# Optimization experiments

Hardware: AMD Instinct MI355X
Metric: run time of the kernel (lower is better)

The kernel has to match this reference:

```python
import jax, jax.numpy as jnp
import numpy as np

B, T, C = 4, 2048, 1024
NH, HS = 16, 64  # num_heads, head_size; NH*HS == C


def setup_inputs() -> dict:
    key = jax.random.key(0)
    ks = jax.random.split(key, 6)
    scale = C ** -0.5
    return {
        "x": jax.random.normal(ks[0], (B, T, C), dtype=jnp.float32),
        "Wk": jax.random.normal(ks[1], (C, C), dtype=jnp.float32) * scale,
        "Wq": jax.random.normal(ks[2], (C, C), dtype=jnp.float32) * scale,
        "Wv": jax.random.normal(ks[3], (C, C), dtype=jnp.float32) * scale,
        "Wp": jax.random.normal(ks[4], (C, C), dtype=jnp.float32) * scale,
        "bp": jax.random.normal(ks[5], (C,), dtype=jnp.float32) * 0.01,
    }


def reference(x, Wk, Wq, Wv, Wp, bp):
    # x: [B, T, C]. Linear(y) = y @ W.T (torch convention), no bias for k/q/v.
    def split_heads(t):
        return t.reshape(B, T, NH, HS).transpose(0, 2, 1, 3)  # [B, NH, T, HS]

    k = split_heads(x @ Wk.T)
    q = split_heads(x @ Wq.T)
    v = split_heads(x @ Wv.T)

    scores = jnp.einsum('bnqh,bnkh->bnqk', q, k) * (HS ** -0.5)  # [B,NH,T,T]
    causal = jnp.tril(jnp.ones((T, T), dtype=bool))
    scores = jnp.where(causal[None, None, :, :], scores, -jnp.inf)
    att = jax.nn.softmax(scores, axis=-1)
    out = jnp.einsum('bnqk,bnkh->bnqh', att, v)  # [B,NH,T,HS]
    out = out.transpose(0, 2, 1, 3).reshape(B, T, C)
    out = out @ Wp.T + bp
    return out
```

## Files before the change

kernel.cpp:

```cpp
#include <hip/hip_runtime.h>
#include <hip/hip_bf16.h>
#include <stdint.h>

typedef unsigned int uint;
typedef unsigned short ushort_t;
typedef unsigned long long ull;

#define B_ 4
#define T_ 2048
#define C_ 1024
#define NH_ 16
#define HS_ 64
#define M_ (B_*T_)

typedef __bf16 bf16x8 __attribute__((ext_vector_type(8)));
typedef float f32x4 __attribute__((ext_vector_type(4)));

__device__ __forceinline__ ushort_t f2bf(float f) {
    uint u = __builtin_bit_cast(uint, f);
    u += 0x7fff + ((u >> 16) & 1);
    return (ushort_t)(u >> 16);
}

__device__ __forceinline__ void gload_lds16(const void* g, void* l) {
    __builtin_amdgcn_global_load_lds((const __attribute__((address_space(1))) void*)g,
                                     (__attribute__((address_space(3))) void*)l, 16, 0, 0);
}

__global__ void convert_bf16(const float* __restrict__ in, ushort_t* __restrict__ out,
                             int n4) {
    int i = blockIdx.x * blockDim.x + threadIdx.x;
    if (i >= n4) return;
    float4 v = ((const float4*)in)[i];
    ushort4 o;
    o.x = f2bf(v.x); o.y = f2bf(v.y); o.z = f2bf(v.z); o.w = f2bf(v.w);
    ((ushort4*)out)[i] = o;
}

__global__ void convert_w4(const float* __restrict__ Wq, const float* __restrict__ Wk,
                           const float* __restrict__ Wv, const float* __restrict__ Wp,
                           ushort_t* __restrict__ wqkv, ushort_t* __restrict__ wp) {
    int i = blockIdx.x * blockDim.x + threadIdx.x;
    int which = blockIdx.y;
    const float* src = (which == 0) ? Wq : (which == 1) ? Wk : (which == 2) ? Wv : Wp;
    ushort_t* dst = (which < 3) ? (wqkv + (size_t)which * C_ * C_) : wp;
    float scale = (which == 0) ? 0.125f * 1.44269504088896f : 1.0f;
    float4 v = ((const float4*)src)[i];
    ushort4 o;
    o.x = f2bf(v.x * scale); o.y = f2bf(v.y * scale);
    o.z = f2bf(v.z * scale); o.w = f2bf(v.w * scale);
    ((ushort4*)dst)[i] = o;
}

template<int MODE>
__global__ __launch_bounds__(256) void gemm_nt(const ushort_t* __restrict__ A,
                                               const ushort_t* __restrict__ Bw,
                                               void* __restrict__ out0,
                                               ushort_t* __restrict__ out1,
                                               ushort_t* __restrict__ out2,
                                               const float* __restrict__ bias) {
    __shared__ __align__(16) ushort_t As[128 * 32];
    __shared__ __align__(16) ushort_t Bs[128 * 32];

    const int tid  = threadIdx.x;
    const int lane = tid & 63;
    const int w    = tid >> 6;
    const int wm   = w >> 1, wn = w & 1;
    const int r16  = lane & 15, g = lane >> 4;
    const int row0 = blockIdx.y * 128;
    const int col0 = blockIdx.x * 128;

    f32x4 acc[4][4] = {};

    for (int kt = 0; kt < C_ / 32; ++kt) {
        const int k0 = kt * 32;
#pragma unroll
        for (int i = 0; i < 2; ++i) {
            int s = i * 256 + w * 64 + lane;
            const ushort_t* ga = A  + (size_t)(row0 + (s >> 2)) * C_ + k0 + (s & 3) * 8;
            const ushort_t* gb = Bw + (size_t)(col0 + (s >> 2)) * C_ + k0 + (s & 3) * 8;
            gload_lds16(ga, &As[(i * 256 + w * 64) * 8]);
            gload_lds16(gb, &Bs[(i * 256 + w * 64) * 8]);
        }
        __syncthreads();

        bf16x8 af[4], bfr[4];
#pragma unroll
        for (int m = 0; m < 4; ++m)
            af[m] = *reinterpret_cast<const bf16x8*>(&As[(wm * 64 + m * 16 + r16) * 32 + g * 8]);
#pragma unroll
        for (int n = 0; n < 4; ++n)
            bfr[n] = *reinterpret_cast<const bf16x8*>(&Bs[(wn * 64 + n * 16 + r16) * 32 + g * 8]);
#pragma unroll
        for (int m = 0; m < 4; ++m)
#pragma unroll
            for (int n = 0; n < 4; ++n)
                acc[m][n] = __builtin_amdgcn_mfma_f32_16x16x32_bf16(af[m], bfr[n], acc[m][n], 0, 0, 0);
        __syncthreads();
    }

#pragma unroll
    for (int m = 0; m < 4; ++m) {
#pragma unroll
        for (int n = 0; n < 4; ++n) {
#pragma unroll
            for (int r = 0; r < 4; ++r) {
                int row = row0 + wm * 64 + m * 16 + g * 4 + r;
                int col = col0 + wn * 64 + n * 16 + r16;
                float val = acc[m][n][r];
                if (MODE == 2) {
                    ((float*)out0)[(size_t)row * C_ + col] = val + bias[col];
                } else {
                    int b = row >> 11, t = row & (T_ - 1);
                    int sect = col >> 10;
                    int c = col & (C_ - 1);
                    int h = c >> 6, hs = c & 63;
                    size_t bh = (size_t)(b * NH_ + h);
                    if (sect == 0)
                        ((ushort_t*)out0)[(bh * T_ + t) * HS_ + hs] = f2bf(val);
                    else if (sect == 1)
                        out1[(bh * T_ + t) * HS_ + hs] = f2bf(val);
                    else
                        out2[(bh * HS_ + hs) * T_ + t] = f2bf(val);
                }
            }
        }
    }
}

__global__ __launch_bounds__(512) void attn_fwd(const ushort_t* __restrict__ q,
                                                const ushort_t* __restrict__ k,
                                                const ushort_t* __restrict__ vT,
                                                ushort_t* __restrict__ o) {
    __shared__ __align__(16) ushort_t Kt[2][64 * 64];
    __shared__ __align__(16) ushort_t Vt[2][64 * 64];
    __shared__ __align__(16) ushort_t Pl[8][16 * 64];

    const int tid  = threadIdx.x;
    const int lane = tid & 63;
    const int w    = tid >> 6;
    const int r16  = lane & 15, g = lane >> 4;
    const int bid  = blockIdx.x;
    const int bh   = bid & 63;
    const int qt   = (T_ / 128 - 1) - (bid >> 6);
    const int qw   = qt * 128 + w * 16;
    const int nt   = 2 * qt + 2;

    const size_t hbase = (size_t)bh * T_ * HS_;

    bf16x8 qf[2];
#pragma unroll
    for (int s = 0; s < 2; ++s)
        qf[s] = *reinterpret_cast<const bf16x8*>(&q[hbase + (size_t)(qw + r16) * HS_ + s * 32 + g * 8]);

    f32x4 oacc[4] = {};
    float lrow[4] = {0.f, 0.f, 0.f, 0.f};

    {
        int s = tid, rr = s >> 3, j = s & 7, jg = j ^ (rr & 7);
        gload_lds16(k  + hbase + (size_t)rr * HS_ + jg * 8, &Kt[0][s * 8]);
        gload_lds16(vT + hbase + (size_t)rr * T_  + jg * 8, &Vt[0][s * 8]);
    }

    for (int kt = 0; kt < nt; ++kt) {
        const int cur = kt & 1;
        const int kb  = kt * 64;

        if (kt + 1 < nt) {
            int kb2 = kb + 64;
            int s = tid, rr = s >> 3, j = s & 7, jg = j ^ (rr & 7);
            gload_lds16(k  + hbase + (size_t)(kb2 + rr) * HS_ + jg * 8, &Kt[cur ^ 1][s * 8]);
            gload_lds16(vT + hbase + (size_t)rr * T_ + kb2 + jg * 8,    &Vt[cur ^ 1][s * 8]);
            asm volatile("s_waitcnt vmcnt(2)" ::: "memory");
        } else {
            asm volatile("s_waitcnt vmcnt(0)" ::: "memory");
        }
        __builtin_amdgcn_s_barrier();
        asm volatile("" ::: "memory");

        if (kb <= qw + 15) {
            f32x4 sacc[4] = {};
            __builtin_amdgcn_s_setprio(1);
#pragma unroll
            for (int n = 0; n < 4; ++n) {
#pragma unroll
                for (int s = 0; s < 2; ++s) {
                    int rowk = n * 16 + r16;
                    int cb = (s * 64 + g * 16) ^ ((rowk & 7) << 4);
                    bf16x8 kf = *reinterpret_cast<const bf16x8*>(
                        reinterpret_cast<const char*>(&Kt[cur][rowk * 64]) + cb);
                    sacc[n] = __builtin_amdgcn_mfma_f32_16x16x32_bf16(qf[s], kf, sacc[n], 0, 0, 0);
                }
            }
            __builtin_amdgcn_s_setprio(0);

            const bool need_mask = (kb + 63 > qw);
            ushort_t* pb = &Pl[w][0];
#pragma unroll
            for (int n = 0; n < 4; ++n) {
#pragma unroll
                for (int r = 0; r < 4; ++r) {
                    float sv = sacc[n][r];
                    if (need_mask) {
                        int kcol = kb + n * 16 + r16;
                        int qrow = qw + g * 4 + r;
                        if (kcol > qrow) sv = -1e30f;
                    }
                    float p = __builtin_amdgcn_exp2f(sv);
                    lrow[r] += p;
                    ushort_t pb16 = (ushort_t)((__builtin_bit_cast(uint, p) + 0x8000u) >> 16);
                    int prow = g * 4 + r;
                    int cb = (n * 32 + r16 * 2) ^ ((prow & 7) << 4);
                    *(ushort_t*)((char*)pb + prow * 128 + cb) = pb16;
                }
            }

            __builtin_amdgcn_s_setprio(1);
#pragma unroll
            for (int s = 0; s < 2; ++s) {
                int cbp = (s * 64 + g * 16) ^ ((r16 & 7) << 4);
                bf16x8 pf = *reinterpret_cast<const bf16x8*>((const char*)pb + r16 * 128 + cbp);
#pragma unroll
                for (int n = 0; n < 4; ++n) {
                    int rowv = n * 16 + r16;
                    int cbv = (s * 64 + g * 16) ^ ((rowv & 7) << 4);
                    bf16x8 vf = *reinterpret_cast<const bf16x8*>(
                        reinterpret_cast<const char*>(&Vt[cur][rowv * 64]) + cbv);
                    oacc[n] = __builtin_amdgcn_mfma_f32_16x16x32_bf16(pf, vf, oacc[n], 0, 0, 0);
                }
            }
            __builtin_amdgcn_s_setprio(0);
        }
        __builtin_amdgcn_s_barrier();
        asm volatile("" ::: "memory");
    }

#pragma unroll
    for (int mk = 1; mk <= 8; mk <<= 1)
#pragma unroll
        for (int r = 0; r < 4; ++r)
            lrow[r] += __shfl_xor(lrow[r], mk, 64);

    const int b = bh >> 4, h = bh & 15;
#pragma unroll
    for (int r = 0; r < 4; ++r) {
        float inv = 1.0f / lrow[r];
        int trow = qw + g * 4 + r;
        size_t obase = ((size_t)(b * T_ + trow) << 10) + h * 64;
#pragma unroll
        for (int n = 0; n < 4; ++n)
            o[obase + n * 16 + r16] = f2bf(oacc[n][r] * inv);
    }
}

extern "C" void kernel_launch(void* const* d_in, const int* in_sizes, int n_in,
                              void* d_out, int out_size, void* d_ws, size_t ws_size,
                              hipStream_t stream) {
    const float* x  = (const float*)d_in[0];
    const float* Wk = (const float*)d_in[1];
    const float* Wq = (const float*)d_in[2];
    const float* Wv = (const float*)d_in[3];
    const float* Wp = (const float*)d_in[4];
    const float* bp = (const float*)d_in[5];
    float* out = (float*)d_out;

    char* ws = (char*)d_ws;
    ushort_t* xbf  = (ushort_t*)(ws);
    ushort_t* wqkv = (ushort_t*)(ws + (size_t)(16 << 20));
    ushort_t* wpbf = (ushort_t*)(ws + (size_t)(22 << 20));
    ushort_t* qb   = (ushort_t*)(ws + (size_t)(24 << 20));
    ushort_t* kb   = (ushort_t*)(ws + (size_t)(40 << 20));
    ushort_t* vtb  = (ushort_t*)(ws + (size_t)(56 << 20));
    ushort_t* aob  = (ushort_t*)(ws + (size_t)(72 << 20));

    {
        int n4 = M_ * C_ / 4;
        convert_bf16<<<dim3((n4 + 255) / 256), dim3(256), 0, stream>>>(x, xbf, n4);
    }
    {
        int n4 = C_ * C_ / 4;
        convert_w4<<<dim3(n4 / 256, 4), dim3(256), 0, stream>>>(Wq, Wk, Wv, Wp, wqkv, wpbf);
    }

    gemm_nt<0><<<dim3(3 * C_ / 128, M_ / 128), 256, 0, stream>>>(xbf, wqkv, qb, kb, vtb, nullptr);

    attn_fwd<<<dim3((T_ / 128) * B_ * NH_), 512, 0, stream>>>(qb, kb, vtb, aob);

    gemm_nt<2><<<dim3(C_ / 128, M_ / 128), 256, 0, stream>>>(aob, wpbf, out, nullptr, nullptr, bp);
}
```

Baseline: 269.3 us.

## Double-buffer GEMM with 128x256 tiles, BK=64, swizzled LDS and 512 threads

Rewrites the bf16 NT GEMM main loop used for both the QKV and output projections. Tiles grow to 128x256 with K-step 64 and 8 waves per block. Global-to-LDS loads for the next K tile are issued before computing on the current one, gated by vmcnt waits and raw barriers. LDS uses an XOR swizzle to avoid bank conflicts, and s_setprio is raised around the MFMA burst. The aim is to hide load latency and cut barriers per FLOP, at the cost of 96KB of LDS per block, which lowers occupancy, and fewer blocks for the output projection.

```diff
diff --git a/kernel.cpp b/kernel.cpp
--- a/kernel.cpp
+++ b/kernel.cpp
@@ -25,6 +25,10 @@
 __device__ __forceinline__ void gload_lds16(const void* g, void* l) {
     __builtin_amdgcn_global_load_lds((const __attribute__((address_space(1))) void*)g,
                                      (__attribute__((address_space(3))) void*)l, 16, 0, 0);
+}
+
+__device__ __forceinline__ f32x4 mfma16(bf16x8 a, bf16x8 b, f32x4 c) {
+    return __builtin_amdgcn_mfma_f32_16x16x32_bf16(a, b, c, 0, 0, 0);
 }
 
 __global__ void convert_bf16(const float* __restrict__ in, ushort_t* __restrict__ out,
@@ -53,50 +57,89 @@
 }
 
 template<int MODE>
-__global__ __launch_bounds__(256) void gemm_nt(const ushort_t* __restrict__ A,
+__global__ __launch_bounds__(512) void gemm_nt(const ushort_t* __restrict__ A,
                                                const ushort_t* __restrict__ Bw,
                                                void* __restrict__ out0,
                                                ushort_t* __restrict__ out1,
                                                ushort_t* __restrict__ out2,
                                                const float* __restrict__ bias) {
-    __shared__ __align__(16) ushort_t As[128 * 32];
-    __shared__ __align__(16) ushort_t Bs[128 * 32];
+    __shared__ __align__(16) ushort_t As[2][128 * 64];
+    __shared__ __align__(16) ushort_t Bs[2][256 * 64];
 
     const int tid  = threadIdx.x;
     const int lane = tid & 63;
     const int w    = tid >> 6;
-    const int wm   = w >> 1, wn = w & 1;
+    const int wm   = w >> 2;
+    const int wn   = w & 3;
     const int r16  = lane & 15, g = lane >> 4;
     const int row0 = blockIdx.y * 128;
-    const int col0 = blockIdx.x * 128;
+    const int col0 = blockIdx.x * 256;
+    const int NK   = C_ / 64;
 
     f32x4 acc[4][4] = {};
 
-    for (int kt = 0; kt < C_ / 32; ++kt) {
-        const int k0 = kt * 32;
-#pragma unroll
-        for (int i = 0; i < 2; ++i) {
-            int s = i * 256 + w * 64 + lane;
-            const ushort_t* ga = A  + (size_t)(row0 + (s >> 2)) * C_ + k0 + (s & 3) * 8;
-            const ushort_t* gb = Bw + (size_t)(col0 + (s >> 2)) * C_ + k0 + (s & 3) * 8;
-            gload_lds16(ga, &As[(i * 256 + w * 64) * 8]);
-            gload_lds16(gb, &Bs[(i * 256 + w * 64) * 8]);
+#pragma unroll
+    for (int i = 0; i < 2; ++i) {
+        int s = i * 512 + tid, row = s >> 3, jg = (s & 7) ^ (row & 7);
+        gload_lds16(A + (size_t)(row0 + row) * C_ + jg * 8, &As[0][s * 8]);
+    }
+#pragma unroll
+    for (int i = 0; i < 4; ++i) {
+        int s = i * 512 + tid, row = s >> 3, jg = (s & 7) ^ (row & 7);
+        gload_lds16(Bw + (size_t)(col0 + row) * C_ + jg * 8, &Bs[0][s * 8]);
+    }
+
+    for (int kt = 0; kt < NK; ++kt) {
+        const int cur = kt & 1;
+        if (kt + 1 < NK) {
+            const int k0 = (kt + 1) * 64;
+#pragma unroll
+            for (int i = 0; i < 2; ++i) {
+                int s = i * 512 + tid, row = s >> 3, jg = (s & 7) ^ (row & 7);
+                gload_lds16(A + (size_t)(row0 + row) * C_ + k0 + jg * 8, &As[cur ^ 1][s * 8]);
+            }
+#pragma unroll
+            for (int i = 0; i < 4; ++i) {
+                int s = i * 512 + tid, row = s >> 3, jg = (s & 7) ^ (row & 7);
+                gload_lds16(Bw + (size_t)(col0 + row) * C_ + k0 + jg * 8, &Bs[cur ^ 1][s * 8]);
+            }
+            asm volatile("s_waitcnt vmcnt(6)" ::: "memory");
+        } else {
+            asm volatile("s_waitcnt vmcnt(0)" ::: "memory");
         }
-        __syncthreads();
-
-        bf16x8 af[4], bfr[4];
+        __builtin_amdgcn_s_barrier();
+        asm volatile("" ::: "memory");
+
+        const char* Ab = (const char*)&As[cur][0];
+        const char* Bb = (const char*)&Bs[cur][0];
+        bf16x8 af[4][2], bfr[4][2];
 #pragma unroll
         for (int m = 0; m < 4; ++m)
-            af[m] = *reinterpret_cast<const bf16x8*>(&As[(wm * 64 + m * 16 + r16) * 32 + g * 8]);
+#pragma unroll
+            for (int sk = 0; sk < 2; ++sk) {
+                int row = wm * 64 + m * 16 + r16;
+                int j = ((sk * 4 + g) ^ (r16 & 7)) * 16;
+                af[m][sk] = *(const bf16x8*)(Ab + row * 128 + j);
+            }
 #pragma unroll
         for (int n = 0; n < 4; ++n)
-            bfr[n] = *reinterpret_cast<const bf16x8*>(&Bs[(wn * 64 + n * 16 + r16) * 32 + g * 8]);
+#pragma unroll
+            for (int sk = 0; sk < 2; ++sk) {
+                int row = wn * 64 + n * 16 + r16;
+                int j = ((sk * 4 + g) ^ (r16 & 7)) * 16;
+                bfr[n][sk] = *(const bf16x8*)(Bb + row * 128 + j);
+            }
+        __builtin_amdgcn_s_setprio(1);
 #pragma unroll
         for (int m = 0; m < 4; ++m)
 #pragma unroll
-            for (int n = 0; n < 4; ++n)
-                acc[m][n] = __builtin_amdgcn_mfma_f32_16x16x32_bf16(af[m], bfr[n], acc[m][n], 0, 0, 0);
-        __syncthreads();
+            for (int n = 0; n < 4; ++n) {
+                acc[m][n] = mfma16(af[m][0], bfr[n][0], acc[m][n]);
+                acc[m][n] = mfma16(af[m][1], bfr[n][1], acc[m][n]);
+            }
+        __builtin_amdgcn_s_setprio(0);
+        __builtin_amdgcn_s_barrier();
+        asm volatile("" ::: "memory");
     }
 
 #pragma unroll
@@ -282,9 +325,9 @@
         convert_w4<<<dim3(n4 / 256, 4), dim3(256), 0, stream>>>(Wq, Wk, Wv, Wp, wqkv, wpbf);
     }
 
-    gemm_nt<0><<<dim3(3 * C_ / 128, M_ / 128), 256, 0, stream>>>(xbf, wqkv, qb, kb, vtb, nullptr);
+    gemm_nt<0><<<dim3(3 * C_ / 256, M_ / 128), 512, 0, stream>>>(xbf, wqkv, qb, kb, vtb, nullptr);
 
     attn_fwd<<<dim3((T_ / 128) * B_ * NH_), 512, 0, stream>>>(qb, kb, vtb, aob);
 
-    gemm_nt<2><<<dim3(C_ / 128, M_ / 128), 256, 0, stream>>>(aob, wpbf, out, nullptr, nullptr, bp);
-}
+    gemm_nt<2><<<dim3(C_ / 256, M_ / 128), 512, 0, stream>>>(aob, wpbf, out, nullptr, nullptr, bp);
+}
```

Result: slower. 289.1 us (+7.3%).

## Pipeline GEMM with 6-stage LDS ring, swizzle, and 128x256 tiles

Applied to the files above, without the earlier changes.

Reworks the bf16 GEMM kernels to use 512-thread blocks computing 128x256 output tiles. Global-to-LDS loads now go through a 6-deep ring buffer with explicit vmcnt waits, so loads for later k-steps overlap MFMA work on the current one. An XOR swizzle on the LDS layout is meant to reduce bank conflicts, and MFMA sections are wrapped in s_setprio. This costs much more LDS per block (about 144KB) and allows only one block per CU, with fewer blocks in the grid.

```diff
diff --git a/kernel.cpp b/kernel.cpp
--- a/kernel.cpp
+++ b/kernel.cpp
@@ -12,6 +12,7 @@
 #define NH_ 16
 #define HS_ 64
 #define M_ (B_*T_)
+#define NBUF 6
 
 typedef __bf16 bf16x8 __attribute__((ext_vector_type(8)));
 typedef float f32x4 __attribute__((ext_vector_type(4)));
@@ -25,6 +26,10 @@
 __device__ __forceinline__ void gload_lds16(const void* g, void* l) {
     __builtin_amdgcn_global_load_lds((const __attribute__((address_space(1))) void*)g,
                                      (__attribute__((address_space(3))) void*)l, 16, 0, 0);
+}
+
+__device__ __forceinline__ f32x4 mfma16(bf16x8 a, bf16x8 b, f32x4 c) {
+    return __builtin_amdgcn_mfma_f32_16x16x32_bf16(a, b, c, 0, 0, 0);
 }
 
 __global__ void convert_bf16(const float* __restrict__ in, ushort_t* __restrict__ out,
@@ -53,51 +58,93 @@
 }
 
 template<int MODE>
-__global__ __launch_bounds__(256) void gemm_nt(const ushort_t* __restrict__ A,
-                                               const ushort_t* __restrict__ Bw,
-                                               void* __restrict__ out0,
-                                               ushort_t* __restrict__ out1,
-                                               ushort_t* __restrict__ out2,
-                                               const float* __restrict__ bias) {
-    __shared__ __align__(16) ushort_t As[128 * 32];
-    __shared__ __align__(16) ushort_t Bs[128 * 32];
+__global__ __launch_bounds__(512, 1) void gemm_nt(const ushort_t* __restrict__ A,
+                                                  const ushort_t* __restrict__ Bw,
+                                                  void* __restrict__ out0,
+                                                  ushort_t* __restrict__ out1,
+                                                  ushort_t* __restrict__ out2,
+                                                  const float* __restrict__ bias) {
+    __shared__ __align__(16) ushort_t As[NBUF][128 * 32];
+    __shared__ __align__(16) ushort_t Bs[NBUF][256 * 32];
 
     const int tid  = threadIdx.x;
     const int lane = tid & 63;
     const int w    = tid >> 6;
-    const int wm   = w >> 1, wn = w & 1;
+    const int wm   = w >> 2;
+    const int wn   = w & 3;
     const int r16  = lane & 15, g = lane >> 4;
     const int row0 = blockIdx.y * 128;
-    const int col0 = blockIdx.x * 128;
+    const int col0 = blockIdx.x * 256;
+    const int NK   = C_ / 32;
 
     f32x4 acc[4][4] = {};
 
-    for (int kt = 0; kt < C_ / 32; ++kt) {
-        const int k0 = kt * 32;
-#pragma unroll
-        for (int i = 0; i < 2; ++i) {
-            int s = i * 256 + w * 64 + lane;
-            const ushort_t* ga = A  + (size_t)(row0 + (s >> 2)) * C_ + k0 + (s & 3) * 8;
-            const ushort_t* gb = Bw + (size_t)(col0 + (s >> 2)) * C_ + k0 + (s & 3) * 8;
-            gload_lds16(ga, &As[(i * 256 + w * 64) * 8]);
-            gload_lds16(gb, &Bs[(i * 256 + w * 64) * 8]);
-        }
-        __syncthreads();
-
-        bf16x8 af[4], bfr[4];
-#pragma unroll
-        for (int m = 0; m < 4; ++m)
-            af[m] = *reinterpret_cast<const bf16x8*>(&As[(wm * 64 + m * 16 + r16) * 32 + g * 8]);
-#pragma unroll
-        for (int n = 0; n < 4; ++n)
-            bfr[n] = *reinterpret_cast<const bf16x8*>(&Bs[(wn * 64 + n * 16 + r16) * 32 + g * 8]);
-#pragma unroll
-        for (int m = 0; m < 4; ++m)
-#pragma unroll
-            for (int n = 0; n < 4; ++n)
-                acc[m][n] = __builtin_amdgcn_mfma_f32_16x16x32_bf16(af[m], bfr[n], acc[m][n], 0, 0, 0);
-        __syncthreads();
-    }
+    const int arow = tid >> 2, aj = tid & 3;
+    const int ajs  = aj ^ ((arow & 3) ^ ((arow >> 2) & 3));
+    const ushort_t* gA = A + (size_t)(row0 + arow) * C_ + ajs * 8;
+
+    const int brow0 = tid >> 2,          bj0 = tid & 3;
+    const int brow1 = (tid + 512) >> 2,  bj1 = tid & 3;
+    const int bjs0  = bj0 ^ ((brow0 & 3) ^ ((brow0 >> 2) & 3));
+    const int bjs1  = bj1 ^ ((brow1 & 3) ^ ((brow1 >> 2) & 3));
+    const ushort_t* gB0 = Bw + (size_t)(col0 + brow0) * C_ + bjs0 * 8;
+    const ushort_t* gB1 = Bw + (size_t)(col0 + brow1) * C_ + bjs1 * 8;
+
+    auto stage = [&](int t, int b) {
+        const int k0 = t * 32;
+        gload_lds16(gA  + k0, &As[b][tid * 8]);
+        gload_lds16(gB0 + k0, &Bs[b][tid * 8]);
+        gload_lds16(gB1 + k0, &Bs[b][(tid + 512) * 8]);
+    };
+
+    auto compute = [&](int b) {
+        const char* Ab = (const char*)&As[b][0];
+        const char* Bb = (const char*)&Bs[b][0];
+        bf16x8 af[4], bfv[4];
+#pragma unroll
+        for (int mf = 0; mf < 4; ++mf) {
+            int row = wm * 64 + mf * 16 + r16;
+            int sw  = g ^ ((row & 3) ^ ((row >> 2) & 3));
+            af[mf] = *(const bf16x8*)(Ab + (row * 4 + sw) * 16);
+        }
+#pragma unroll
+        for (int nf = 0; nf < 4; ++nf) {
+            int row = wn * 64 + nf * 16 + r16;
+            int sw  = g ^ ((row & 3) ^ ((row >> 2) & 3));
+            bfv[nf] = *(const bf16x8*)(Bb + (row * 4 + sw) * 16);
+        }
+        __builtin_amdgcn_s_setprio(1);
+#pragma unroll
+        for (int mf = 0; mf < 4; ++mf)
+#pragma unroll
+            for (int nf = 0; nf < 4; ++nf)
+                acc[mf][nf] = mfma16(af[mf], bfv[nf], acc[mf][nf]);
+        __builtin_amdgcn_s_setprio(0);
+    };
+
+#pragma unroll
+    for (int p = 0; p < 5; ++p) stage(p, p);
+
+    int bcur = 0, bstg = 5, tstage = 5;
+
+#define GSTEP(VMIMM) do {                                                    \
+        __builtin_amdgcn_s_barrier();                                        \
+        asm volatile("" ::: "memory");                                       \
+        if (tstage < NK) {                                                   \
+            stage(tstage, bstg);                                             \
+            bstg = (bstg + 1 == NBUF) ? 0 : bstg + 1;                        \
+        }                                                                    \
+        ++tstage;                                                            \
+        asm volatile("s_waitcnt vmcnt(" #VMIMM ")" ::: "memory");            \
+        __builtin_amdgcn_s_barrier();                                        \
+        asm volatile("" ::: "memory");                                       \
+        compute(bcur);                                                       \
+        bcur = (bcur + 1 == NBUF) ? 0 : bcur + 1;                            \
+    } while (0)
+
+    for (int t = 0; t < NK - 5; ++t) GSTEP(15);
+    GSTEP(12); GSTEP(9); GSTEP(6); GSTEP(3); GSTEP(0);
+#undef GSTEP
 
 #pragma unroll
     for (int m = 0; m < 4; ++m) {
@@ -282,9 +329,9 @@
         convert_w4<<<dim3(n4 / 256, 4), dim3(256), 0, stream>>>(Wq, Wk, Wv, Wp, wqkv, wpbf);
     }
 
-    gemm_nt<0><<<dim3(3 * C_ / 128, M_ / 128), 256, 0, stream>>>(xbf, wqkv, qb, kb, vtb, nullptr);
+    gemm_nt<0><<<dim3(3 * C_ / 256, M_ / 128), 512, 0, stream>>>(xbf, wqkv, qb, kb, vtb, nullptr);
 
     attn_fwd<<<dim3((T_ / 128) * B_ * NH_), 512, 0, stream>>>(qb, kb, vtb, aob);
 
-    gemm_nt<2><<<dim3(C_ / 128, M_ / 128), 256, 0, stream>>>(aob, wpbf, out, nullptr, nullptr, bp);
-}
+    gemm_nt<2><<<dim3(C_ / 256, M_ / 128), 512, 0, stream>>>(aob, wpbf, out, nullptr, nullptr, bp);
+}
```

New measurement: 312.8 us. 1.16x slower.

## Double-buffer GEMM LDS tiles with XOR swizzle and prefetch overlap

Applied to the files above, without the earlier changes.

The NT GEMM now keeps two LDS buffers and issues the direct-to-LDS global loads for the next K tile before computing the current one. It waits with vmcnt counters instead of a full sync. It also XOR-swizzles the 16-byte chunk index within each LDS row to cut bank conflicts on fragment reads, and raises wave priority around the MFMA block. This doubles LDS use per block, which may lower occupancy, and relies on hand-placed waitcnt and barriers being correct.

```diff
diff --git a/kernel.cpp b/kernel.cpp
--- a/kernel.cpp
+++ b/kernel.cpp
@@ -25,6 +25,10 @@
 __device__ __forceinline__ void gload_lds16(const void* g, void* l) {
     __builtin_amdgcn_global_load_lds((const __attribute__((address_space(1))) void*)g,
                                      (__attribute__((address_space(3))) void*)l, 16, 0, 0);
+}
+
+__device__ __forceinline__ f32x4 mfma16(bf16x8 a, bf16x8 b, f32x4 c) {
+    return __builtin_amdgcn_mfma_f32_16x16x32_bf16(a, b, c, 0, 0, 0);
 }
 
 __global__ void convert_bf16(const float* __restrict__ in, ushort_t* __restrict__ out,
@@ -59,8 +63,8 @@
                                                ushort_t* __restrict__ out1,
                                                ushort_t* __restrict__ out2,
                                                const float* __restrict__ bias) {
-    __shared__ __align__(16) ushort_t As[128 * 32];
-    __shared__ __align__(16) ushort_t Bs[128 * 32];
+    __shared__ __align__(16) ushort_t As[2][128 * 32];
+    __shared__ __align__(16) ushort_t Bs[2][128 * 32];
 
     const int tid  = threadIdx.x;
     const int lane = tid & 63;
@@ -69,34 +73,63 @@
     const int r16  = lane & 15, g = lane >> 4;
     const int row0 = blockIdx.y * 128;
     const int col0 = blockIdx.x * 128;
+    const int NK   = C_ / 32;
 
     f32x4 acc[4][4] = {};
 
-    for (int kt = 0; kt < C_ / 32; ++kt) {
-        const int k0 = kt * 32;
-#pragma unroll
-        for (int i = 0; i < 2; ++i) {
-            int s = i * 256 + w * 64 + lane;
-            const ushort_t* ga = A  + (size_t)(row0 + (s >> 2)) * C_ + k0 + (s & 3) * 8;
-            const ushort_t* gb = Bw + (size_t)(col0 + (s >> 2)) * C_ + k0 + (s & 3) * 8;
-            gload_lds16(ga, &As[(i * 256 + w * 64) * 8]);
-            gload_lds16(gb, &Bs[(i * 256 + w * 64) * 8]);
-        }
-        __syncthreads();
-
-        bf16x8 af[4], bfr[4];
-#pragma unroll
-        for (int m = 0; m < 4; ++m)
-            af[m] = *reinterpret_cast<const bf16x8*>(&As[(wm * 64 + m * 16 + r16) * 32 + g * 8]);
-#pragma unroll
-        for (int n = 0; n < 4; ++n)
-            bfr[n] = *reinterpret_cast<const bf16x8*>(&Bs[(wn * 64 + n * 16 + r16) * 32 + g * 8]);
-#pragma unroll
-        for (int m = 0; m < 4; ++m)
-#pragma unroll
-            for (int n = 0; n < 4; ++n)
-                acc[m][n] = __builtin_amdgcn_mfma_f32_16x16x32_bf16(af[m], bfr[n], acc[m][n], 0, 0, 0);
-        __syncthreads();
+    const int s0 = tid, s1 = tid + 256;
+    const int ar0 = s0 >> 2, aj0 = (s0 & 3) ^ ((ar0 >> 1) & 3);
+    const int ar1 = s1 >> 2, aj1 = (s1 & 3) ^ ((ar1 >> 1) & 3);
+    const ushort_t* gA0 = A  + (size_t)(row0 + ar0) * C_ + aj0 * 8;
+    const ushort_t* gA1 = A  + (size_t)(row0 + ar1) * C_ + aj1 * 8;
+    const ushort_t* gB0 = Bw + (size_t)(col0 + ar0) * C_ + aj0 * 8;
+    const ushort_t* gB1 = Bw + (size_t)(col0 + ar1) * C_ + aj1 * 8;
+
+    auto stage = [&](int t, int b) {
+        const int k0 = t * 32;
+        gload_lds16(gA0 + k0, &As[b][s0 * 8]);
+        gload_lds16(gA1 + k0, &As[b][s1 * 8]);
+        gload_lds16(gB0 + k0, &Bs[b][s0 * 8]);
+        gload_lds16(gB1 + k0, &Bs[b][s1 * 8]);
+    };
+
+    stage(0, 0);
+
+    for (int kt = 0; kt < NK; ++kt) {
+        const int cur = kt & 1;
+        if (kt + 1 < NK) {
+            stage(kt + 1, cur ^ 1);
+            asm volatile("s_waitcnt vmcnt(4)" ::: "memory");
+        } else {
+            asm volatile("s_waitcnt vmcnt(0)" ::: "memory");
+        }
+        __builtin_amdgcn_s_barrier();
+        asm volatile("" ::: "memory");
+
+        const char* Ab = (const char*)&As[cur][0];
+        const char* Bb = (const char*)&Bs[cur][0];
+        bf16x8 af[4], bfv[4];
+#pragma unroll
+        for (int mf = 0; mf < 4; ++mf) {
+            int row = wm * 64 + mf * 16 + r16;
+            int js  = g ^ ((row >> 1) & 3);
+            af[mf] = *(const bf16x8*)(Ab + row * 64 + js * 16);
+        }
+#pragma unroll
+        for (int nf = 0; nf < 4; ++nf) {
+            int row = wn * 64 + nf * 16 + r16;
+            int js  = g ^ ((row >> 1) & 3);
+            bfv[nf] = *(const bf16x8*)(Bb + row * 64 + js * 16);
+        }
+        __builtin_amdgcn_s_setprio(1);
+#pragma unroll
+        for (int mf = 0; mf < 4; ++mf)
+#pragma unroll
+            for (int nf = 0; nf < 4; ++nf)
+                acc[mf][nf] = mfma16(af[mf], bfv[nf], acc[mf][nf]);
+        __builtin_amdgcn_s_setprio(0);
+        __builtin_amdgcn_s_barrier();
+        asm volatile("" ::: "memory");
     }
 
 #pragma unroll
```

Result: slower. 282.0 us (+4.7%).
